# Performance work log

Hardware: AMD Instinct MI355X
Metric: run time of the kernel (lower is better)

## Reference

```python
import jax, jax.numpy as jnp
import numpy as np

POOL = 16  # in_downsampling == internal_downsampling == 16


def _conv1x1(x, w, b):
    # x: [B,C,H,W], w: [O,C], b: [O] -> [B,O,H,W]
    return jnp.einsum('oc,bchw->bohw', w, x) + b[None, :, None, None]


def _maxpool(x, k):
    return jax.lax.reduce_window(x, -jnp.inf, jax.lax.max,
                                 (1, 1, k, k), (1, 1, k, k), 'VALID')


def setup_inputs() -> dict:
    key = jax.random.key(0)
    ks = jax.random.split(key, 7)
    B, C, Ci, H, W = 4, 256, 128, 256, 256
    s_in = 1.0 / np.sqrt(C)
    return {
        'x':   jax.random.normal(ks[0], (B, C, H, W), jnp.float32),
        'f_w': jax.random.normal(ks[1], (Ci, C), jnp.float32) * s_in,
        'f_b': jax.random.normal(ks[2], (Ci,), jnp.float32) * 0.01,
        'g_w': jax.random.normal(ks[3], (Ci, C), jnp.float32) * s_in,
        'g_b': jax.random.normal(ks[4], (Ci,), jnp.float32) * 0.01,
        'h_w': jax.random.normal(ks[5], (C, C), jnp.float32) * s_in,
        'h_b': jax.random.normal(ks[6], (C,), jnp.float32) * 0.01,
    }


def reference(x, f_w, f_b, g_w, g_b, h_w, h_b):
    B, C, H, W = x.shape
    # pooled query / key features: [B, Ci, h1, w1] and [B, Ci, h2, w2]
    fv = _maxpool(_conv1x1(x, f_w, f_b), POOL)
    gv = _maxpool(_conv1x1(x, g_w, g_b), POOL)
    # dots[b,i,j,k,l] = sum_c fv[b,c,i,j] * gv[b,c,k,l]  (channel dot-product)
    dots = jnp.einsum('bcij,bckl->bijkl', fv, gv)
    Bd, h1, w1, h2, w2 = dots.shape
    # exp=True path: softmax over the flattened (h2, w2) key positions
    dots = jax.nn.softmax(dots.reshape(Bd, h1, w1, h2 * w2), axis=-1)
    dots = dots.reshape(Bd, h1, w1, h2, w2)
    # pooled values: [B, C, h2, w2]
    hv = _maxpool(_conv1x1(x, h_w, h_b), POOL)
    # weighted sum over key positions -> [B, C, h1, w1]
    out = jnp.einsum('bijkl,bckl->bcij', dots, hv)
    # bilinear upsample (align_corners=False == half-pixel, matches jax resize)
    up = jax.image.resize(out, (B, C, H, W), method='bilinear')
    return up + x
```

## Files before the change

kernel.cpp:

```cpp
#include <hip/hip_runtime.h>
#include <hip/hip_fp16.h>

typedef _Float16 f16;
typedef _Float16 f16x2_t __attribute__((ext_vector_type(2)));
typedef _Float16 f16x8_t __attribute__((ext_vector_type(8)));
typedef float    f32x4_t __attribute__((ext_vector_type(4)));

#define NB  4
#define NC  256
#define NH  256
#define NW  256

__global__ __launch_bounds__(256) void k_convert_w(
    const float* __restrict__ f_w, const float* __restrict__ g_w,
    const float* __restrict__ h_w, f16* __restrict__ wf)
{
    int id = blockIdx.x * 256 + threadIdx.x;
    int cout = id >> 8;
    float v;
    if (cout < 128)       v = f_w[id];
    else if (cout < 256)  v = g_w[id - 128*256];
    else                  v = h_w[id - 256*256];
    wf[id] = (f16)v;
}

__global__ __launch_bounds__(1024, 4) void k_pooled_conv(
    const float* __restrict__ x, const f16* __restrict__ wf,
    const float* __restrict__ f_b, const float* __restrict__ g_b,
    const float* __restrict__ h_b,
    float* __restrict__ pooled_fg,
    float* __restrict__ pooledT_h)
{
    __shared__ __align__(16) char smem[65536];

    const int t    = threadIdx.x;
    const int wave = t >> 6;
    const int lane = t & 63;
    const int l15  = lane & 15;
    const int lg   = lane >> 4;
    const bool isfg = (wave < 8);
    const int coutbase = isfg ? wave * 32 : 256 + (wave - 8) * 32;

    f16x8_t bfrag[2][8];
    #pragma unroll
    for (int nn = 0; nn < 2; nn++) {
        const f16* wr = wf + (coutbase + nn*16 + l15) * 256 + lg*8;
        #pragma unroll
        for (int k = 0; k < 8; k++)
            bfrag[nn][k] = *(const f16x8_t*)(wr + k*32);
    }
    float biasv[2];
    #pragma unroll
    for (int nn = 0; nn < 2; nn++) {
        int c = coutbase + nn*16 + l15;
        biasv[nn] = (c < 128) ? f_b[c] : (c < 256) ? g_b[c - 128] : h_b[c - 256];
    }

    const int ct  = t >> 3;
    const int c0  = ct * 2;
    const int pt  = t & 7;
    const int pl0 = pt * 4;
    const int sm  = pt >> 2;
    const int kw  = c0 >> 5, lgw = (c0 >> 3) & 3, jw = c0 & 7;
    unsigned woff[4];
    #pragma unroll
    for (int w = 0; w < 4; w++) {
        int p15 = (pl0 & 15) + w;
        unsigned g = (unsigned)((p15 >> 2) | ((lgw & 1) << 2) | ((p15 & 3) << 3) | ((lgw >> 1) << 5));
        woff[w] = ((unsigned)(sm * 8 + kw) << 10) + g * 16 + (unsigned)jw * 2;
    }
    const unsigned rdg =
        (unsigned)((l15 >> 2) | ((lg & 1) << 2) | ((l15 & 3) << 3) | ((lg >> 1) << 5)) * 16u;

    const int bid   = blockIdx.x;
    const int b     = bid >> 6;
    const int wbase = bid * 4;
    const float* xb = x + (size_t)b * (256u * 65536u);
    const int dyl = pl0 >> 4;
    const int dxl = pl0 & 15;

    float vmax[2] = {-3.0e38f, -3.0e38f};

    auto loadst = [&](int gsd, float4& A0, float4& A1) {
        int win = wbase + (gsd >> 3);
        int s   = gsd & 7;
        int wi = (win >> 4) & 15, wj = win & 15;
        const float* src = xb + (size_t)c0 * 65536u
                         + (unsigned)((wi*16 + s*2 + dyl) * 256 + wj*16 + dxl);
        A0 = *(const float4*)src;
        A1 = *(const float4*)(src + 65536);
    };
    auto writest = [&](const float4& A0, const float4& A1, int buf) {
        char* base = smem + buf * 32768;
        const float* a0 = (const float*)&A0;
        const float* a1 = (const float*)&A1;
        #pragma unroll
        for (int w = 0; w < 4; w++) {
            float v0 = a0[w], v1 = a1[w];
            f16 h0 = (f16)v0, h1 = (f16)v1;
            f16x2_t hv = {h0, h1};
            f16x2_t lv = {(f16)(v0 - (float)h0), (f16)(v1 - (float)h1)};
            *(f16x2_t*)(base + woff[w])         = hv;
            *(f16x2_t*)(base + 16384 + woff[w]) = lv;
        }
    };
    auto mfmast = [&](int buf) {
        const char* base = smem + buf * 32768;
        if (isfg) {
            #pragma unroll
            for (int m = 0; m < 2; m++) {
                f32x4_t acc0 = {0.f,0.f,0.f,0.f}, acc1 = {0.f,0.f,0.f,0.f};
                #pragma unroll
                for (int k = 0; k < 8; k++) {
                    const char* p = base + ((m*8 + k) << 10) + rdg;
                    f16x8_t ah = *(const f16x8_t*)p;
                    f16x8_t al = *(const f16x8_t*)(p + 16384);
                    acc0 = __builtin_amdgcn_mfma_f32_16x16x32_f16(ah, bfrag[0][k], acc0, 0,0,0);
                    acc1 = __builtin_amdgcn_mfma_f32_16x16x32_f16(ah, bfrag[1][k], acc1, 0,0,0);
                    acc0 = __builtin_amdgcn_mfma_f32_16x16x32_f16(al, bfrag[0][k], acc0, 0,0,0);
                    acc1 = __builtin_amdgcn_mfma_f32_16x16x32_f16(al, bfrag[1][k], acc1, 0,0,0);
                }
                #pragma unroll
                for (int r = 0; r < 4; r++) {
                    vmax[0] = fmaxf(vmax[0], acc0[r]);
                    vmax[1] = fmaxf(vmax[1], acc1[r]);
                }
            }
        } else {
            #pragma unroll
            for (int m = 0; m < 2; m++) {
                f32x4_t acc0 = {0.f,0.f,0.f,0.f}, acc1 = {0.f,0.f,0.f,0.f};
                #pragma unroll
                for (int k = 0; k < 8; k++) {
                    const char* p = base + ((m*8 + k) << 10) + rdg;
                    f16x8_t ah = *(const f16x8_t*)p;
                    acc0 = __builtin_amdgcn_mfma_f32_16x16x32_f16(ah, bfrag[0][k], acc0, 0,0,0);
                    acc1 = __builtin_amdgcn_mfma_f32_16x16x32_f16(ah, bfrag[1][k], acc1, 0,0,0);
                }
                #pragma unroll
                for (int r = 0; r < 4; r++) {
                    vmax[0] = fmaxf(vmax[0], acc0[r]);
                    vmax[1] = fmaxf(vmax[1], acc1[r]);
                }
            }
        }
    };
    auto finalize = [&](int win) {
        int wn = win & 255;
        #pragma unroll
        for (int nn = 0; nn < 2; nn++) {
            float v = vmax[nn];
            v = fmaxf(v, __shfl_xor(v, 16, 64));
            v = fmaxf(v, __shfl_xor(v, 32, 64));
            if (lane < 16) {
                float val = v + biasv[nn];
                int c = coutbase + nn*16 + lane;
                if (isfg) pooled_fg[((b*256 + c)  << 8) + wn] = val;
                else      pooledT_h[((b*256 + wn) << 8) + (c - 256)] = val;
            }
            vmax[nn] = -3.0e38f;
        }
    };

    float4 rA0, rA1, rB0, rB1;
    loadst(0, rA0, rA1);
    writest(rA0, rA1, 0);
    loadst(1, rB0, rB1);
    __syncthreads();

    #pragma unroll 1
    for (int gs = 0; gs < 32; gs += 2) {
        if (gs + 2 < 32) loadst(gs + 2, rA0, rA1);
        writest(rB0, rB1, 1);
        mfmast(0);
        __syncthreads();
        if (gs + 3 < 32) loadst(gs + 3, rB0, rB1);
        if (gs + 2 < 32) writest(rA0, rA1, 0);
        mfmast(1);
        if ((gs & 7) == 6) finalize(wbase + (gs >> 3));
        __syncthreads();
    }
}

__global__ __launch_bounds__(256) void k_attn(
    const float* __restrict__ pooled_fg, const float* __restrict__ pooledT_h,
    float* __restrict__ attnout)
{
    __shared__ float red[4];
    __shared__ float p_lds[256];
    const int blk = blockIdx.x;
    const int b = blk >> 8;
    const int q = blk & 255;
    const int t = threadIdx.x;

    const float* fv = pooled_fg + ((b*256) << 8) + q;
    const float* gv = pooled_fg + ((b*256 + 128) << 8) + t;

    float s = 0.f;
    #pragma unroll 8
    for (int c = 0; c < 128; c++)
        s += fv[c << 8] * gv[c << 8];

    float m = s;
    #pragma unroll
    for (int o = 1; o < 64; o <<= 1) m = fmaxf(m, __shfl_xor(m, o, 64));
    if ((t & 63) == 0) red[t >> 6] = m;
    __syncthreads();
    m = fmaxf(fmaxf(red[0], red[1]), fmaxf(red[2], red[3]));
    __syncthreads();

    float p = expf(s - m);
    float sum = p;
    #pragma unroll
    for (int o = 1; o < 64; o <<= 1) sum += __shfl_xor(sum, o, 64);
    if ((t & 63) == 0) red[t >> 6] = sum;
    __syncthreads();
    sum = red[0] + red[1] + red[2] + red[3];
    p /= sum;
    p_lds[t] = p;
    __syncthreads();

    const float* hv = pooledT_h + (b << 16) + t;
    float acc = 0.f;
    #pragma unroll 8
    for (int k = 0; k < 256; k++)
        acc += p_lds[k] * hv[k << 8];
    attnout[((b*256 + t) << 8) + q] = acc;
}

__global__ __launch_bounds__(256) void k_upsample_add(
    const float* __restrict__ x, const float* __restrict__ attnout,
    float* __restrict__ out)
{
    __shared__ float L[256];
    const int blk = blockIdx.x;
    const int t = threadIdx.x;
    L[t] = attnout[(blk << 8) + t];
    __syncthreads();
    const float* xp = x   + (size_t)blk * 65536;
    float*       op = out + (size_t)blk * 65536;

    const int x4 = (t & 63) << 2;
    const int yo = t >> 6;
    float fxv[4]; int x0v[4], x1v[4];
    #pragma unroll
    for (int e = 0; e < 4; e++) {
        float sx  = (x4 + e + 0.5f) * 0.0625f - 0.5f;
        float x0f = floorf(sx);
        fxv[e] = sx - x0f;
        int ix0 = (int)x0f;
        x0v[e] = min(15, max(0, ix0));
        x1v[e] = min(15, max(0, ix0 + 1));
    }
    for (int it = 0; it < 64; it++) {
        int y = it*4 + yo;
        float sy  = (y + 0.5f) * 0.0625f - 0.5f;
        float y0f = floorf(sy);
        float fy  = sy - y0f;
        int iy0 = (int)y0f;
        int y0 = min(15, max(0, iy0));
        int y1 = min(15, max(0, iy0 + 1));
        const float* Ly0 = L + y0*16;
        const float* Ly1 = L + y1*16;
        float4 xin = *(const float4*)(xp + y*256 + x4);
        float o[4]; const float* xe = (const float*)&xin;
        #pragma unroll
        for (int e = 0; e < 4; e++) {
            float top = Ly0[x0v[e]] + fxv[e] * (Ly0[x1v[e]] - Ly0[x0v[e]]);
            float bot = Ly1[x0v[e]] + fxv[e] * (Ly1[x1v[e]] - Ly1[x0v[e]]);
            o[e] = top + fy * (bot - top) + xe[e];
        }
        float4 ov = make_float4(o[0], o[1], o[2], o[3]);
        *(float4*)(op + y*256 + x4) = ov;
    }
}

extern "C" void kernel_launch(void* const* d_in, const int* in_sizes, int n_in,
                              void* d_out, int out_size, void* d_ws, size_t ws_size,
                              hipStream_t stream)
{
    const float* x   = (const float*)d_in[0];
    const float* f_w = (const float*)d_in[1];
    const float* f_b = (const float*)d_in[2];
    const float* g_w = (const float*)d_in[3];
    const float* g_b = (const float*)d_in[4];
    const float* h_w = (const float*)d_in[5];
    const float* h_b = (const float*)d_in[6];
    float* out = (float*)d_out;

    char* ws = (char*)d_ws;
    f16*   wf        = (f16*)ws;
    float* pooled_fg = (float*)(ws + (256<<10));
    float* pooledT_h = (float*)(ws + (256<<10) + (1<<20));
    float* attnout   = (float*)(ws + (256<<10) + (2<<20));

    k_convert_w   <<<512, 256, 0, stream>>>(f_w, g_w, h_w, wf);
    k_pooled_conv <<<256, 1024, 0, stream>>>(x, wf, f_b, g_b, h_b, pooled_fg, pooledT_h);
    k_attn        <<<1024, 256, 0, stream>>>(pooled_fg, pooledT_h, attnout);
    k_upsample_add<<<1024, 256, 0, stream>>>(x, attnout, out);
}
```

Baseline: 283.8 us.

## Widen per-wave conv tile to 64 outputs with 512-thread blocks and strided loads

The pooled conv kernel drops from 1024 to 512 threads per block. Each wave now computes 64 output channels (4 MFMA column tiles) instead of 32, so every LDS A-fragment read is reused across twice as many MFMAs. The global load pattern changes from float4 vectors to scalar strided loads over 4 channels, and each thread writes 8-byte f16x4 LDS stores. The risks are higher register pressure from 32 B-fragments and 16 staged floats, fewer waves to hide latency, and less coalesced global loads.

```diff
diff --git a/kernel.cpp b/kernel.cpp
--- a/kernel.cpp
+++ b/kernel.cpp
@@ -2,7 +2,7 @@
 #include <hip/hip_fp16.h>
 
 typedef _Float16 f16;
-typedef _Float16 f16x2_t __attribute__((ext_vector_type(2)));
+typedef _Float16 f16x4_t __attribute__((ext_vector_type(4)));
 typedef _Float16 f16x8_t __attribute__((ext_vector_type(8)));
 typedef float    f32x4_t __attribute__((ext_vector_type(4)));
 
@@ -24,7 +24,7 @@
     wf[id] = (f16)v;
 }
 
-__global__ __launch_bounds__(1024, 4) void k_pooled_conv(
+__global__ __launch_bounds__(512, 2) void k_pooled_conv(
     const float* __restrict__ x, const f16* __restrict__ wf,
     const float* __restrict__ f_b, const float* __restrict__ g_b,
     const float* __restrict__ h_b,
@@ -38,144 +38,128 @@
     const int lane = t & 63;
     const int l15  = lane & 15;
     const int lg   = lane >> 4;
-    const bool isfg = (wave < 8);
-    const int coutbase = isfg ? wave * 32 : 256 + (wave - 8) * 32;
-
-    f16x8_t bfrag[2][8];
-    #pragma unroll
-    for (int nn = 0; nn < 2; nn++) {
-        const f16* wr = wf + (coutbase + nn*16 + l15) * 256 + lg*8;
+    const bool isfg = (wave < 4);
+    const int coutbase = wave * 64;
+
+    f16x8_t bfrag[4][8];
+    #pragma unroll
+    for (int n = 0; n < 4; n++) {
+        const f16* wr = wf + (coutbase + n*16 + l15) * 256 + lg*8;
         #pragma unroll
         for (int k = 0; k < 8; k++)
-            bfrag[nn][k] = *(const f16x8_t*)(wr + k*32);
-    }
-    float biasv[2];
-    #pragma unroll
-    for (int nn = 0; nn < 2; nn++) {
-        int c = coutbase + nn*16 + l15;
-        biasv[nn] = (c < 128) ? f_b[c] : (c < 256) ? g_b[c - 128] : h_b[c - 256];
-    }
-
-    const int ct  = t >> 3;
-    const int c0  = ct * 2;
-    const int pt  = t & 7;
-    const int pl0 = pt * 4;
-    const int sm  = pt >> 2;
-    const int kw  = c0 >> 5, lgw = (c0 >> 3) & 3, jw = c0 & 7;
+            bfrag[n][k] = *(const f16x8_t*)(wr + k*32);
+    }
+    float biasv[4];
+    #pragma unroll
+    for (int n = 0; n < 4; n++) {
+        int c = coutbase + n*16 + l15;
+        biasv[n] = (c < 128) ? f_b[c] : (c < 256) ? g_b[c - 128] : h_b[c - 256];
+    }
+
+    const int q   = t & 3;
+    const int dyl = (t >> 2) & 1;
+    const int c0  = (t >> 3) * 4;
     unsigned woff[4];
     #pragma unroll
     for (int w = 0; w < 4; w++) {
-        int p15 = (pl0 & 15) + w;
-        unsigned g = (unsigned)((p15 >> 2) | ((lgw & 1) << 2) | ((p15 & 3) << 3) | ((lgw >> 1) << 5));
-        woff[w] = ((unsigned)(sm * 8 + kw) << 10) + g * 16 + (unsigned)jw * 2;
-    }
-    const unsigned rdg =
-        (unsigned)((l15 >> 2) | ((lg & 1) << 2) | ((l15 & 3) << 3) | ((lg >> 1) << 5)) * 16u;
+        int dx = q + 4*w;
+        unsigned lslot = (unsigned)(dx | (((c0 >> 3) & 3) << 4));
+        woff[w] = ((unsigned)(dyl*8 + (c0 >> 5)) << 10) + lslot*16u + (unsigned)((c0 & 4) * 2);
+    }
 
     const int bid   = blockIdx.x;
     const int b     = bid >> 6;
     const int wbase = bid * 4;
     const float* xb = x + (size_t)b * (256u * 65536u);
-    const int dyl = pl0 >> 4;
-    const int dxl = pl0 & 15;
-
-    float vmax[2] = {-3.0e38f, -3.0e38f};
-
-    auto loadst = [&](int gsd, float4& A0, float4& A1) {
+
+    float vmax[4] = {-3.0e38f, -3.0e38f, -3.0e38f, -3.0e38f};
+
+    auto loadst = [&](int gsd, float* r) {
         int win = wbase + (gsd >> 3);
         int s   = gsd & 7;
         int wi = (win >> 4) & 15, wj = win & 15;
         const float* src = xb + (size_t)c0 * 65536u
-                         + (unsigned)((wi*16 + s*2 + dyl) * 256 + wj*16 + dxl);
-        A0 = *(const float4*)src;
-        A1 = *(const float4*)(src + 65536);
-    };
-    auto writest = [&](const float4& A0, const float4& A1, int buf) {
+                         + (unsigned)((wi*16 + s*2 + dyl) * 256 + wj*16 + q);
+        #pragma unroll
+        for (int cc = 0; cc < 4; cc++)
+            #pragma unroll
+            for (int w = 0; w < 4; w++)
+                r[cc*4 + w] = src[(unsigned)cc * 65536u + (unsigned)w * 4u];
+    };
+    auto writest = [&](const float* r, int buf) {
         char* base = smem + buf * 32768;
-        const float* a0 = (const float*)&A0;
-        const float* a1 = (const float*)&A1;
         #pragma unroll
         for (int w = 0; w < 4; w++) {
-            float v0 = a0[w], v1 = a1[w];
-            f16 h0 = (f16)v0, h1 = (f16)v1;
-            f16x2_t hv = {h0, h1};
-            f16x2_t lv = {(f16)(v0 - (float)h0), (f16)(v1 - (float)h1)};
-            *(f16x2_t*)(base + woff[w])         = hv;
-            *(f16x2_t*)(base + 16384 + woff[w]) = lv;
+            f16x4_t hv, lv;
+            #pragma unroll
+            for (int cc = 0; cc < 4; cc++) {
+                float v = r[cc*4 + w];
+                f16 h = (f16)v;
+                hv[cc] = h;
+                lv[cc] = (f16)(v - (float)h);
+            }
+            *(f16x4_t*)(base + woff[w])         = hv;
+            *(f16x4_t*)(base + 16384 + woff[w]) = lv;
         }
     };
     auto mfmast = [&](int buf) {
-        const char* base = smem + buf * 32768;
-        if (isfg) {
-            #pragma unroll
-            for (int m = 0; m < 2; m++) {
-                f32x4_t acc0 = {0.f,0.f,0.f,0.f}, acc1 = {0.f,0.f,0.f,0.f};
+        const char* base = smem + buf * 32768 + lane * 16;
+        #pragma unroll
+        for (int m = 0; m < 2; m++) {
+            f32x4_t acc[4] = {{0.f,0.f,0.f,0.f},{0.f,0.f,0.f,0.f},
+                              {0.f,0.f,0.f,0.f},{0.f,0.f,0.f,0.f}};
+            #pragma unroll
+            for (int k = 0; k < 8; k++) {
+                const char* p = base + ((m*8 + k) << 10);
+                f16x8_t ah = *(const f16x8_t*)p;
                 #pragma unroll
-                for (int k = 0; k < 8; k++) {
-                    const char* p = base + ((m*8 + k) << 10) + rdg;
-                    f16x8_t ah = *(const f16x8_t*)p;
+                for (int n = 0; n < 4; n++)
+                    acc[n] = __builtin_amdgcn_mfma_f32_16x16x32_f16(ah, bfrag[n][k], acc[n], 0,0,0);
+                if (isfg) {
                     f16x8_t al = *(const f16x8_t*)(p + 16384);
-                    acc0 = __builtin_amdgcn_mfma_f32_16x16x32_f16(ah, bfrag[0][k], acc0, 0,0,0);
-                    acc1 = __builtin_amdgcn_mfma_f32_16x16x32_f16(ah, bfrag[1][k], acc1, 0,0,0);
-                    acc0 = __builtin_amdgcn_mfma_f32_16x16x32_f16(al, bfrag[0][k], acc0, 0,0,0);
-                    acc1 = __builtin_amdgcn_mfma_f32_16x16x32_f16(al, bfrag[1][k], acc1, 0,0,0);
-                }
-                #pragma unroll
-                for (int r = 0; r < 4; r++) {
-                    vmax[0] = fmaxf(vmax[0], acc0[r]);
-                    vmax[1] = fmaxf(vmax[1], acc1[r]);
+                    #pragma unroll
+                    for (int n = 0; n < 4; n++)
+                        acc[n] = __builtin_amdgcn_mfma_f32_16x16x32_f16(al, bfrag[n][k], acc[n], 0,0,0);
                 }
             }
-        } else {
-            #pragma unroll
-            for (int m = 0; m < 2; m++) {
-                f32x4_t acc0 = {0.f,0.f,0.f,0.f}, acc1 = {0.f,0.f,0.f,0.f};
+            #pragma unroll
+            for (int n = 0; n < 4; n++)
                 #pragma unroll
-                for (int k = 0; k < 8; k++) {
-                    const char* p = base + ((m*8 + k) << 10) + rdg;
-                    f16x8_t ah = *(const f16x8_t*)p;
-                    acc0 = __builtin_amdgcn_mfma_f32_16x16x32_f16(ah, bfrag[0][k], acc0, 0,0,0);
-                    acc1 = __builtin_amdgcn_mfma_f32_16x16x32_f16(ah, bfrag[1][k], acc1, 0,0,0);
-                }
-                #pragma unroll
-                for (int r = 0; r < 4; r++) {
-                    vmax[0] = fmaxf(vmax[0], acc0[r]);
-                    vmax[1] = fmaxf(vmax[1], acc1[r]);
-                }
-            }
+                for (int r = 0; r < 4; r++)
+                    vmax[n] = fmaxf(vmax[n], acc[n][r]);
         }
     };
     auto finalize = [&](int win) {
         int wn = win & 255;
         #pragma unroll
-        for (int nn = 0; nn < 2; nn++) {
-            float v = vmax[nn];
+        for (int n = 0; n < 4; n++) {
+            float v = vmax[n];
             v = fmaxf(v, __shfl_xor(v, 16, 64));
             v = fmaxf(v, __shfl_xor(v, 32, 64));
             if (lane < 16) {
-                float val = v + biasv[nn];
-                int c = coutbase + nn*16 + lane;
+                float val = v + biasv[n];
+                int c = coutbase + n*16 + lane;
                 if (isfg) pooled_fg[((b*256 + c)  << 8) + wn] = val;
                 else      pooledT_h[((b*256 + wn) << 8) + (c - 256)] = val;
             }
-            vmax[nn] = -3.0e38f;
-        }
-    };
-
-    float4 rA0, rA1, rB0, rB1;
-    loadst(0, rA0, rA1);
-    writest(rA0, rA1, 0);
-    loadst(1, rB0, rB1);
+            vmax[n] = -3.0e38f;
+        }
+    };
+
+    float rA[16], rB[16];
+    loadst(0, rA);
+    writest(rA, 0);
+    loadst(1, rB);
     __syncthreads();
 
     #pragma unroll 1
     for (int gs = 0; gs < 32; gs += 2) {
-        if (gs + 2 < 32) loadst(gs + 2, rA0, rA1);
-        writest(rB0, rB1, 1);
+        if (gs + 2 < 32) loadst(gs + 2, rA);
+        writest(rB, 1);
         mfmast(0);
         __syncthreads();
-        if (gs + 3 < 32) loadst(gs + 3, rB0, rB1);
-        if (gs + 2 < 32) writest(rA0, rA1, 0);
+        if (gs + 3 < 32) loadst(gs + 3, rB);
+        if (gs + 2 < 32) writest(rA, 0);
         mfmast(1);
         if ((gs & 7) == 6) finalize(wbase + (gs >> 3));
         __syncthreads();
@@ -295,7 +279,7 @@
     float* attnout   = (float*)(ws + (256<<10) + (2<<20));
 
     k_convert_w   <<<512, 256, 0, stream>>>(f_w, g_w, h_w, wf);
-    k_pooled_conv <<<256, 1024, 0, stream>>>(x, wf, f_b, g_b, h_b, pooled_fg, pooledT_h);
+    k_pooled_conv <<<256, 512, 0, stream>>>(x, wf, f_b, g_b, h_b, pooled_fg, pooledT_h);
     k_attn        <<<1024, 256, 0, stream>>>(pooled_fg, pooledT_h, attnout);
     k_upsample_add<<<1024, 256, 0, stream>>>(x, attnout, out);
 }
```

After: 305.9 us. 1.08x slower.
